# Performance work log

Measured on AMD Instinct MI355X. Metric: run time of the kernel, lower is better.

The kernel has to match this reference:

```python
import jax, jax.numpy as jnp
import numpy as np

B, LATENT = 8192, 1024
NR, NC = 12, 12                      # nb_rows, nb_cols
H0, W0 = NR + 2, NC + 2              # 14x14 after reshape
EPS = 1e-5
SLOPE = 0.01                         # LeakyReLU default


def setup_inputs() -> dict:
    key = jax.random.key(0)
    ks = jax.random.split(key, 9)
    s = 0.05
    return {
        "x": jax.random.normal(ks[0], (B, LATENT), jnp.float32),
        "fc_w": jax.random.normal(ks[1], (H0 * W0 * 36, LATENT), jnp.float32) * s,
        "fc_b": jax.random.normal(ks[2], (H0 * W0 * 36,), jnp.float32) * s,
        "conv_w": jax.random.normal(ks[3], (16, 36, 2, 2), jnp.float32) * s,
        "conv_b": jax.random.normal(ks[4], (16,), jnp.float32) * s,
        "gamma": jnp.ones((16,), jnp.float32),
        "beta": jnp.zeros((16,), jnp.float32),
        # locally-connected weights: (out_ch, in_ch, Hout, Wout, k*k)
        "lw1": jax.random.normal(ks[5], (6, 16, H0 - 1, W0 - 1, 4), jnp.float32) * s,
        "lw2": jax.random.normal(ks[6], (1, 6, H0 - 2, W0 - 2, 4), jnp.float32) * s,
    }


def _leaky(x):
    return jnp.where(x >= 0, x, SLOPE * x)


def _local_conv2(x, w):
    # x: (B,C,H,W); w: (O,C,Ho,Wo,4) with k=2, stride 1, no padding
    Ho, Wo = w.shape[2], w.shape[3]
    patches = jnp.stack(
        [x[:, :, dy:dy + Ho, dx:dx + Wo] for dy in (0, 1) for dx in (0, 1)],
        axis=-1)  # (B,C,Ho,Wo,4)
    return jnp.einsum('bchwk,ochwk->bohw', patches, w)


def reference(x, fc_w, fc_b, conv_w, conv_b, gamma, beta, lw1, lw2):
    # fc -> view(B, H0, W0, 36) -> permute to NCHW
    h = x @ fc_w.T + fc_b
    h = h.reshape(B, H0, W0, 36).transpose(0, 3, 1, 2)  # (B,36,14,14)
    # Conv2d k=2 padding='same' (torch pads bottom/right for even kernels)
    h = jax.lax.conv_general_dilated(
        h, conv_w, window_strides=(1, 1), padding=((0, 1), (0, 1)),
        dimension_numbers=('NCHW', 'OIHW', 'NCHW')) + conv_b[None, :, None, None]
    h = _leaky(h)
    # BatchNorm2d (training mode: batch stats, biased var)
    mu = h.mean(axis=(0, 2, 3), keepdims=True)
    var = h.var(axis=(0, 2, 3), keepdims=True)
    h = (h - mu) * jax.lax.rsqrt(var + EPS)
    h = h * gamma[None, :, None, None] + beta[None, :, None, None]
    # locally-connected stack: 14x14 -> 13x13 -> 12x12
    h = _leaky(_local_conv2(h, lw1))
    return _local_conv2(h, lw2)  # (B,1,12,12)
```

## Files before the change

### kernel.cpp

```cpp
#include <hip/hip_runtime.h>


#define SLOPE 0.01f

typedef __bf16 bf16x8 __attribute__((ext_vector_type(8)));
typedef float f32x4 __attribute__((ext_vector_type(4)));

typedef const __attribute__((address_space(1))) void* gas_ptr;
typedef __attribute__((address_space(3))) void* las_ptr;

__device__ __forceinline__ void load16_to_lds(const void* g, void* l) {
  __builtin_amdgcn_global_load_lds((gas_ptr)g, (las_ptr)l, 16, 0, 0);
}

__device__ __forceinline__ unsigned short f2bf(float f) {
  union { float f; unsigned int u; } v; v.f = f;
  unsigned int r = v.u + 0x7FFFu + ((v.u >> 16) & 1u);
  return (unsigned short)(r >> 16);
}
__device__ __forceinline__ float bfbits2f(unsigned int bits16) {
  union { unsigned int u; float f; } v; v.u = bits16 << 16;
  return v.f;
}
__device__ __forceinline__ float leaky(float v) { return v >= 0.f ? v : SLOPE * v; }

__global__ void k_cast_x(const float* __restrict__ x, unsigned short* __restrict__ xb,
                         float* __restrict__ stats) {
  if (blockIdx.x == 0 && threadIdx.x < 32) stats[threadIdx.x] = 0.f;
  int gid = blockIdx.x * 256 + threadIdx.x;
  const float4* x4 = (const float4*)x;
  float4 a = x4[gid * 2], b = x4[gid * 2 + 1];
  union { unsigned short s[8]; uint4 v; } o;
  o.s[0] = f2bf(a.x); o.s[1] = f2bf(a.y); o.s[2] = f2bf(a.z); o.s[3] = f2bf(a.w);
  o.s[4] = f2bf(b.x); o.s[5] = f2bf(b.y); o.s[6] = f2bf(b.z); o.s[7] = f2bf(b.w);
  ((uint4*)xb)[gid] = o.v;
}

__global__ void k_fold(const float* __restrict__ fc_w, const float* __restrict__ fc_b,
                       const float* __restrict__ conv_w, const float* __restrict__ conv_b,
                       unsigned short* __restrict__ Wc, float* __restrict__ bc) {
  __shared__ float cw[2304];
  int blk = blockIdx.x, og = blockIdx.y, t = threadIdx.x;
  if (blk == 196) {
    if (og != 0) return;
    uint4 z = make_uint4(0, 0, 0, 0);
    uint4* dst = (uint4*)(Wc + 3136 * 1024);
    for (int i = t; i < 8192; i += 256) dst[i] = z;
    for (int i = 3136 + t; i < 3200; i += 256) bc[i] = 0.f;
    return;
  }
  for (int i = t; i < 2304; i += 256) cw[i] = conv_w[i];
  __syncthreads();
  int i0 = blk / 14, j0 = blk - (blk / 14) * 14;
  float acc[4][4];
#pragma unroll
  for (int o = 0; o < 4; o++)
#pragma unroll
    for (int q = 0; q < 4; q++) acc[o][q] = 0.f;
  for (int c = 0; c < 36; c++) {
#pragma unroll
    for (int dy = 0; dy < 2; dy++) {
      int ii = i0 + dy; if (ii > 13) continue;
#pragma unroll
      for (int dx = 0; dx < 2; dx++) {
        int jj = j0 + dx; if (jj > 13) continue;
        int row = (ii * 14 + jj) * 36 + c;
        float4 f = *(const float4*)(fc_w + row * 1024 + t * 4);
        int kk = dy * 2 + dx;
#pragma unroll
        for (int oo = 0; oo < 4; oo++) {
          int o = og * 4 + oo;
          float w = cw[(o * 36 + c) * 4 + kk];
          acc[oo][0] += w * f.x; acc[oo][1] += w * f.y;
          acc[oo][2] += w * f.z; acc[oo][3] += w * f.w;
        }
      }
    }
  }
#pragma unroll
  for (int oo = 0; oo < 4; oo++) {
    int o = og * 4 + oo;
    int n = o * 196 + i0 * 14 + j0;
    union { unsigned short s[4]; uint2 v; } u;
    u.s[0] = f2bf(acc[oo][0]); u.s[1] = f2bf(acc[oo][1]);
    u.s[2] = f2bf(acc[oo][2]); u.s[3] = f2bf(acc[oo][3]);
    *(uint2*)(Wc + n * 1024 + t * 4) = u.v;
  }
  if (og == 0 && t < 16) {
    int o = t;
    float b = conv_b[o];
    for (int c = 0; c < 36; c++)
      for (int dy = 0; dy < 2; dy++) {
        int ii = i0 + dy; if (ii > 13) continue;
        for (int dx = 0; dx < 2; dx++) {
          int jj = j0 + dx; if (jj > 13) continue;
          b += cw[(o * 36 + c) * 4 + dy * 2 + dx] * fc_b[(ii * 14 + jj) * 36 + c];
        }
      }
    bc[o * 196 + i0 * 14 + j0] = b;
  }
}

__global__ __launch_bounds__(256, 4) void k_gemm(const unsigned short* __restrict__ Xb,
                                                 const unsigned short* __restrict__ Wcb,
                                                 const float* __restrict__ bc,
                                                 unsigned short* __restrict__ h2,
                                                 float* __restrict__ stats) {
  __shared__ __align__(16) char lds[16384];
  __shared__ float red[4][4];
  const int t = threadIdx.x;
  const int w = t >> 6, lane = t & 63;
  const int quad = lane >> 4, l15 = lane & 15;
  const int bid = blockIdx.x;
  const int xcd = bid & 7, j = bid >> 3;
  const int mblk = xcd * 8 + (j & 7);
  const int nblk = j >> 3;
  const int m0 = mblk * 128, n0 = nblk * 128;
  const int mrow = t & 127, tko = t >> 7;
  const unsigned short* ga = Xb + (m0 + mrow) * 1024 + tko * 8;
  const unsigned short* gb = Wcb + (n0 + mrow) * 1024 + tko * 8;
  char* lA = lds;
  char* lB = lds + 8192;
  const int wbase = w * 1024;
  const int wm0 = (w >> 1) * 64, wn0 = (w & 1) * 64;

  f32x4 acc[4][4];
#pragma unroll
  for (int a = 0; a < 4; a++)
#pragma unroll
    for (int b = 0; b < 4; b++) acc[a][b] = (f32x4){0.f, 0.f, 0.f, 0.f};

  for (int kb = 0; kb < 1024; kb += 32) {
    __syncthreads();
    load16_to_lds(ga + kb,      lA + wbase);
    load16_to_lds(ga + kb + 16, lA + 4096 + wbase);
    load16_to_lds(gb + kb,      lB + wbase);
    load16_to_lds(gb + kb + 16, lB + 4096 + wbase);
    __syncthreads();

    bf16x8 af[4], bfr[4];
#pragma unroll
    for (int mb = 0; mb < 4; mb++)
      af[mb] = *(const bf16x8*)(lA + quad * 2048 + (wm0 + mb * 16 + l15) * 16);
#pragma unroll
    for (int nb = 0; nb < 4; nb++)
      bfr[nb] = *(const bf16x8*)(lB + quad * 2048 + (wn0 + nb * 16 + l15) * 16);
#pragma unroll
    for (int mb = 0; mb < 4; mb++)
#pragma unroll
      for (int nb = 0; nb < 4; nb++)
        acc[mb][nb] = __builtin_amdgcn_mfma_f32_16x16x32_bf16(af[mb], bfr[nb], acc[mb][nb], 0, 0, 0);
  }

  const int cLo = n0 / 196;
  const int cHi = (n0 + 127) / 196;
  float ss0 = 0.f, ss1 = 0.f, sq0 = 0.f, sq1 = 0.f;
#pragma unroll
  for (int nb = 0; nb < 4; nb++) {
    int col = n0 + wn0 + nb * 16 + l15;
    float bias = bc[col];
    int ch = col / 196;
    bool hi = (ch != cLo);
    bool valid = col < 3136;
    float cs = 0.f, cq = 0.f;
#pragma unroll
    for (int mb = 0; mb < 4; mb++) {
#pragma unroll
      for (int r = 0; r < 4; r++) {
        int row = m0 + wm0 + mb * 16 + quad * 4 + r;
        float v = leaky(acc[mb][nb][r] + bias);
        h2[row * 3200 + col] = f2bf(v);
        cs += v; cq += v * v;
      }
    }
    if (valid) {
      if (hi) { ss1 += cs; sq1 += cq; } else { ss0 += cs; sq0 += cq; }
    }
  }
#pragma unroll
  for (int off = 1; off < 64; off <<= 1) {
    ss0 += __shfl_xor(ss0, off, 64);
    ss1 += __shfl_xor(ss1, off, 64);
    sq0 += __shfl_xor(sq0, off, 64);
    sq1 += __shfl_xor(sq1, off, 64);
  }
  if (lane == 0) { red[w][0] = ss0; red[w][1] = ss1; red[w][2] = sq0; red[w][3] = sq1; }
  __syncthreads();
  if (t == 0) {
    float a0 = red[0][0] + red[1][0] + red[2][0] + red[3][0];
    float a1 = red[0][1] + red[1][1] + red[2][1] + red[3][1];
    float b0 = red[0][2] + red[1][2] + red[2][2] + red[3][2];
    float b1 = red[0][3] + red[1][3] + red[2][3] + red[3][3];
    atomicAdd(&stats[cLo], a0);
    atomicAdd(&stats[16 + cLo], b0);
    if (cHi != cLo && cHi < 16) {
      atomicAdd(&stats[cHi], a1);
      atomicAdd(&stats[16 + cHi], b1);
    }
  }
}

__global__ __launch_bounds__(256) void k_tail(const unsigned short* __restrict__ h2,
                                              const float* __restrict__ stats,
                                              const float* __restrict__ gamma,
                                              const float* __restrict__ beta,
                                              const float* __restrict__ lw1,
                                              const float* __restrict__ lw2,
                                              float* __restrict__ out) {
  __shared__ unsigned short h3[4 * 3138];
  __shared__ float h4[4 * 1015];
  __shared__ float sc[16], sh[16];
  int b0 = blockIdx.x * 4, t = threadIdx.x;
  if (t < 16) {
    const float inv = 1.f / 1605632.f;
    float mean = stats[t] * inv;
    float var = stats[16 + t] * inv - mean * mean;
    float rstd = rsqrtf(var + 1e-5f);
    float s = gamma[t] * rstd;
    sc[t] = s; sh[t] = beta[t] - mean * s;
  }
  __syncthreads();
  for (int i = t; i < 6272; i += 256) {
    int bb = i / 1568, q = i - bb * 1568;
    int n = q * 2, o = n / 196;
    unsigned int u = *(const unsigned int*)(h2 + (b0 + bb) * 3200 + n);
    float v0 = bfbits2f(u & 0xffffu) * sc[o] + sh[o];
    float v1 = bfbits2f(u >> 16) * sc[o] + sh[o];
    unsigned int pk = (unsigned int)f2bf(v0) | ((unsigned int)f2bf(v1) << 16);
    *(unsigned int*)(h3 + bb * 3138 + n) = pk;
  }
  __syncthreads();
  for (int u = t; u < 312; u += 256) {
    int bb = u & 3, rest = u >> 2;
    int o = rest / 13, y = rest - o * 13;
    float acc[13];
#pragma unroll
    for (int x = 0; x < 13; x++) acc[x] = 0.f;
    const unsigned short* hb = h3 + bb * 3138;
    for (int c = 0; c < 16; c++) {
      float r0[14], r1[14];
      const unsigned int* p0 = (const unsigned int*)(hb + c * 196 + y * 14);
      const unsigned int* p1 = (const unsigned int*)(hb + c * 196 + (y + 1) * 14);
#pragma unroll
      for (int q = 0; q < 7; q++) {
        unsigned int v0 = p0[q], v1 = p1[q];
        r0[2 * q] = bfbits2f(v0 & 0xffffu); r0[2 * q + 1] = bfbits2f(v0 >> 16);
        r1[2 * q] = bfbits2f(v1 & 0xffffu); r1[2 * q + 1] = bfbits2f(v1 >> 16);
      }
      const float4* wp4 = (const float4*)(lw1 + (((o * 16 + c) * 13 + y) * 13) * 4);
#pragma unroll
      for (int x = 0; x < 13; x++) {
        float4 wv = wp4[x];
        acc[x] += r0[x] * wv.x + r0[x + 1] * wv.y +
                  r1[x] * wv.z + r1[x + 1] * wv.w;
      }
    }
#pragma unroll
    for (int x = 0; x < 13; x++)
      h4[bb * 1015 + (o * 13 + y) * 13 + x] = leaky(acc[x]);
  }
  __syncthreads();
  for (int oi = t; oi < 576; oi += 256) {
    int pos = oi >> 2, bb = oi & 3;
    int y = pos / 12, x = pos - y * 12;
    float a = 0.f;
    const float* hp = h4 + bb * 1015;
    const float4* w4 = (const float4*)lw2;
#pragma unroll
    for (int c = 0; c < 6; c++) {
      float4 wv = w4[(c * 12 + y) * 12 + x];
      int hb = c * 169 + y * 13 + x;
      a += hp[hb] * wv.x + hp[hb + 1] * wv.y +
           hp[hb + 13] * wv.z + hp[hb + 14] * wv.w;
    }
    out[(b0 + bb) * 144 + pos] = a;
  }
}

extern "C" void kernel_launch(void* const* d_in, const int* in_sizes, int n_in,
                              void* d_out, int out_size, void* d_ws, size_t ws_size,
                              hipStream_t stream) {
  const float* x      = (const float*)d_in[0];
  const float* fc_w   = (const float*)d_in[1];
  const float* fc_b   = (const float*)d_in[2];
  const float* conv_w = (const float*)d_in[3];
  const float* conv_b = (const float*)d_in[4];
  const float* gamma  = (const float*)d_in[5];
  const float* beta   = (const float*)d_in[6];
  const float* lw1    = (const float*)d_in[7];
  const float* lw2    = (const float*)d_in[8];

  char* ws = (char*)d_ws;
  unsigned short* Xb    = (unsigned short*)(ws);
  unsigned short* Wc    = (unsigned short*)(ws + 16777216);
  float*          bc    = (float*)(ws + 23330816);
  float*          stats = (float*)(ws + 23343616);
  unsigned short* h2    = (unsigned short*)(ws + 23343744);

  k_cast_x<<<4096, 256, 0, stream>>>(x, Xb, stats);
  k_fold<<<dim3(197, 4), 256, 0, stream>>>(fc_w, fc_b, conv_w, conv_b, Wc, bc);
  k_gemm<<<1600, 256, 0, stream>>>(Xb, Wc, bc, h2, stats);
  k_tail<<<2048, 256, 0, stream>>>(h2, stats, gamma, beta, lw1, lw2, (float*)d_out);
}
```

Before: 371.9 us.

## Double GEMM K-tile to 64 and restructure weight-fold kernel over K groups

```diff
diff --git a/kernel.cpp b/kernel.cpp
--- a/kernel.cpp
+++ b/kernel.cpp
@@ -40,9 +40,9 @@
                        const float* __restrict__ conv_w, const float* __restrict__ conv_b,
                        unsigned short* __restrict__ Wc, float* __restrict__ bc) {
   __shared__ float cw[2304];
-  int blk = blockIdx.x, og = blockIdx.y, t = threadIdx.x;
+  int blk = blockIdx.x, kg = blockIdx.y, t = threadIdx.x;
   if (blk == 196) {
-    if (og != 0) return;
+    if (kg != 0) return;
     uint4 z = make_uint4(0, 0, 0, 0);
     uint4* dst = (uint4*)(Wc + 3136 * 1024);
     for (int i = t; i < 8192; i += 256) dst[i] = z;
@@ -52,11 +52,10 @@
   for (int i = t; i < 2304; i += 256) cw[i] = conv_w[i];
   __syncthreads();
   int i0 = blk / 14, j0 = blk - (blk / 14) * 14;
-  float acc[4][4];
-#pragma unroll
-  for (int o = 0; o < 4; o++)
-#pragma unroll
-    for (int q = 0; q < 4; q++) acc[o][q] = 0.f;
+  int kcol = kg * 256 + t;
+  float acc[16];
+#pragma unroll
+  for (int o = 0; o < 16; o++) acc[o] = 0.f;
   for (int c = 0; c < 36; c++) {
 #pragma unroll
     for (int dy = 0; dy < 2; dy++) {
@@ -65,28 +64,20 @@
       for (int dx = 0; dx < 2; dx++) {
         int jj = j0 + dx; if (jj > 13) continue;
         int row = (ii * 14 + jj) * 36 + c;
-        float4 f = *(const float4*)(fc_w + row * 1024 + t * 4);
+        float f = fc_w[row * 1024 + kcol];
         int kk = dy * 2 + dx;
 #pragma unroll
-        for (int oo = 0; oo < 4; oo++) {
-          int o = og * 4 + oo;
-          float w = cw[(o * 36 + c) * 4 + kk];
-          acc[oo][0] += w * f.x; acc[oo][1] += w * f.y;
-          acc[oo][2] += w * f.z; acc[oo][3] += w * f.w;
-        }
-      }
-    }
-  }
-#pragma unroll
-  for (int oo = 0; oo < 4; oo++) {
-    int o = og * 4 + oo;
+        for (int o = 0; o < 16; o++)
+          acc[o] += cw[(o * 36 + c) * 4 + kk] * f;
+      }
+    }
+  }
+#pragma unroll
+  for (int o = 0; o < 16; o++) {
     int n = o * 196 + i0 * 14 + j0;
-    union { unsigned short s[4]; uint2 v; } u;
-    u.s[0] = f2bf(acc[oo][0]); u.s[1] = f2bf(acc[oo][1]);
-    u.s[2] = f2bf(acc[oo][2]); u.s[3] = f2bf(acc[oo][3]);
-    *(uint2*)(Wc + n * 1024 + t * 4) = u.v;
-  }
-  if (og == 0 && t < 16) {
+    Wc[n * 1024 + kcol] = f2bf(acc[o]);
+  }
+  if (kg == 0 && t < 16) {
     int o = t;
     float b = conv_b[o];
     for (int c = 0; c < 36; c++)
@@ -106,7 +97,7 @@
                                                  const float* __restrict__ bc,
                                                  unsigned short* __restrict__ h2,
                                                  float* __restrict__ stats) {
-  __shared__ __align__(16) char lds[16384];
+  __shared__ __align__(16) char lds[32768];
   __shared__ float red[4][4];
   const int t = threadIdx.x;
   const int w = t >> 6, lane = t & 63;
@@ -120,7 +111,7 @@
   const unsigned short* ga = Xb + (m0 + mrow) * 1024 + tko * 8;
   const unsigned short* gb = Wcb + (n0 + mrow) * 1024 + tko * 8;
   char* lA = lds;
-  char* lB = lds + 8192;
+  char* lB = lds + 16384;
   const int wbase = w * 1024;
   const int wm0 = (w >> 1) * 64, wn0 = (w & 1) * 64;
 
@@ -130,26 +121,30 @@
 #pragma unroll
     for (int b = 0; b < 4; b++) acc[a][b] = (f32x4){0.f, 0.f, 0.f, 0.f};
 
-  for (int kb = 0; kb < 1024; kb += 32) {
+  for (int kb = 0; kb < 1024; kb += 64) {
     __syncthreads();
-    load16_to_lds(ga + kb,      lA + wbase);
-    load16_to_lds(ga + kb + 16, lA + 4096 + wbase);
-    load16_to_lds(gb + kb,      lB + wbase);
-    load16_to_lds(gb + kb + 16, lB + 4096 + wbase);
+#pragma unroll
+    for (int i = 0; i < 4; i++) {
+      load16_to_lds(ga + kb + i * 16, lA + i * 4096 + wbase);
+      load16_to_lds(gb + kb + i * 16, lB + i * 4096 + wbase);
+    }
     __syncthreads();
 
-    bf16x8 af[4], bfr[4];
-#pragma unroll
-    for (int mb = 0; mb < 4; mb++)
-      af[mb] = *(const bf16x8*)(lA + quad * 2048 + (wm0 + mb * 16 + l15) * 16);
-#pragma unroll
-    for (int nb = 0; nb < 4; nb++)
-      bfr[nb] = *(const bf16x8*)(lB + quad * 2048 + (wn0 + nb * 16 + l15) * 16);
-#pragma unroll
-    for (int mb = 0; mb < 4; mb++)
+#pragma unroll
+    for (int kk = 0; kk < 2; kk++) {
+      bf16x8 af[4], bfr[4];
+#pragma unroll
+      for (int mb = 0; mb < 4; mb++)
+        af[mb] = *(const bf16x8*)(lA + (kk * 4 + quad) * 2048 + (wm0 + mb * 16 + l15) * 16);
 #pragma unroll
       for (int nb = 0; nb < 4; nb++)
-        acc[mb][nb] = __builtin_amdgcn_mfma_f32_16x16x32_bf16(af[mb], bfr[nb], acc[mb][nb], 0, 0, 0);
+        bfr[nb] = *(const bf16x8*)(lB + (kk * 4 + quad) * 2048 + (wn0 + nb * 16 + l15) * 16);
+#pragma unroll
+      for (int mb = 0; mb < 4; mb++)
+#pragma unroll
+        for (int nb = 0; nb < 4; nb++)
+          acc[mb][nb] = __builtin_amdgcn_mfma_f32_16x16x32_bf16(af[mb], bfr[nb], acc[mb][nb], 0, 0, 0);
+    }
   }
 
   const int cLo = n0 / 196;
```

Measured after the change: 384.3 us. +3.3%, slower.
